# Optimization experiments

Hardware: AMD Instinct MI355X
Metric: run time of the kernel (lower is better)

Reference implementation:

```python
import jax, jax.numpy as jnp
from jax import lax
import numpy as np

N, C, H, W = 8, 128, 96, 96
G, K = 8, 3                      # groups, kernel_size
GC = C // G                      # group channels = 16
STRIDE, PAD, DIL = 1, 1, 1
OFFSET_SCALE = 1.0
OM_DIM = int(np.ceil(G * K * K * 3 / 8) * 8)   # 216 (== G*K*K*3, no padding)
GN_EPS = 1e-5


def setup_inputs() -> dict:
    key = jax.random.key(0)
    ks = jax.random.split(key, 7)
    inp = {
        "input": jax.random.normal(ks[0], (N, C, H, W), dtype=jnp.float32),
        # depthwise conv (Conv2d groups=C): OIHW with I=1
        "dw_w": jax.random.normal(ks[1], (C, 1, K, K), dtype=jnp.float32) * 0.1,
        "dw_b": jax.random.normal(ks[2], (C,), dtype=jnp.float32) * 0.05,
        # GroupNorm(num_groups=1) affine params
        "gn_w": jnp.ones((C,), dtype=jnp.float32),
        "gn_b": jnp.zeros((C,), dtype=jnp.float32),
        # offset_mask Linear (module zero-inits; use small random for a meaningful test)
        "om_w": jax.random.normal(ks[3], (OM_DIM, C), dtype=jnp.float32) * 0.02,
        "om_b": jax.random.normal(ks[4], (OM_DIM,), dtype=jnp.float32) * 0.02,
    }
    return inp


def _dcnv4_forward(x, dw_w, dw_b, gn_w, gn_b, om_w, om_b):
    # x: (N, C, H, W)
    # ---- offset/mask branch: depthwise conv -> GroupNorm(1) -> GELU -> Linear
    x1 = lax.conv_general_dilated(
        x, dw_w, window_strides=(1, 1), padding=[(1, 1), (1, 1)],
        feature_group_count=C, dimension_numbers=("NCHW", "OIHW", "NCHW"))
    x1 = x1 + dw_b[None, :, None, None]
    mu = jnp.mean(x1, axis=(1, 2, 3), keepdims=True)
    var = jnp.var(x1, axis=(1, 2, 3), keepdims=True)
    x1 = (x1 - mu) * lax.rsqrt(var + GN_EPS)
    x1 = x1 * gn_w[None, :, None, None] + gn_b[None, :, None, None]
    x1 = jax.nn.gelu(x1, approximate=False)
    x1 = jnp.transpose(x1, (0, 2, 3, 1))                     # (N,H,W,C)
    om = jnp.einsum("nhwc,oc->nhwo", x1, om_w) + om_b        # (N,H,W,216)

    K2 = K * K
    om = om[..., : G * K2 * 3].reshape(N, H, W, G, K2 * 3)
    offs = om[..., : 2 * K2].reshape(N, H, W, G, K2, 2)      # (dx, dy) per point
    mask = om[..., 2 * K2:]                                  # (N,H,W,G,K2), no softmax in DCNv4

    # ---- sampling locations (pixel coords in the unpadded input, zeros outside)
    ky, kx = jnp.meshgrid(jnp.arange(K), jnp.arange(K), indexing="ij")
    base_y = ((ky - (K - 1) / 2.0) * DIL).reshape(-1).astype(jnp.float32)  # (K2,)
    base_x = ((kx - (K - 1) / 2.0) * DIL).reshape(-1).astype(jnp.float32)
    ctr_y = jnp.arange(H, dtype=jnp.float32) * STRIDE - PAD + DIL * (K - 1) / 2.0
    ctr_x = jnp.arange(W, dtype=jnp.float32) * STRIDE - PAD + DIL * (K - 1) / 2.0
    loc_y = ctr_y[None, :, None, None, None] + (base_y + offs[..., 1]) * OFFSET_SCALE
    loc_x = ctr_x[None, None, :, None, None] + (base_x + offs[..., 0]) * OFFSET_SCALE

    # ---- grouped bilinear gather
    xv = jnp.transpose(x, (0, 2, 3, 1)).reshape(N, H, W, G, GC)   # values, channels-last
    y0 = jnp.floor(loc_y)
    x0 = jnp.floor(loc_x)
    ly = loc_y - y0
    lx = loc_x - x0
    y0i = y0.astype(jnp.int32)
    x0i = x0.astype(jnp.int32)
    n_idx = jnp.arange(N)[:, None, None, None, None]
    g_idx = jnp.arange(G)[None, None, None, :, None]

    def gather(yi, xi):
        valid = (yi >= 0) & (yi < H) & (xi >= 0) & (xi < W)
        yc = jnp.clip(yi, 0, H - 1)
        xc = jnp.clip(xi, 0, W - 1)
        v = xv[n_idx, yc, xc, g_idx]                 # (N,H,W,G,K2,GC)
        return v * valid[..., None].astype(xv.dtype)

    samp = (gather(y0i,     x0i)     * ((1 - ly) * (1 - lx))[..., None]
          + gather(y0i,     x0i + 1) * ((1 - ly) * lx)[..., None]
          + gather(y0i + 1, x0i)     * (ly * (1 - lx))[..., None]
          + gather(y0i + 1, x0i + 1) * (ly * lx)[..., None])

    out = jnp.sum(samp * mask[..., None], axis=4)    # (N,H,W,G,GC)
    out = out.reshape(N, H, W, C)
    return jnp.transpose(out, (0, 3, 1, 2))          # (N,C,H,W)


def reference(input, dw_w, dw_b, gn_w, gn_b, om_w, om_b):
    return _dcnv4_forward(input, dw_w, dw_b, gn_w, gn_b, om_w, om_b)
```

## Files before the change

kernel.cpp:

```cpp
#include <hip/hip_runtime.h>

#define N_   8
#define C_   128
#define H_   96
#define W_   96
#define G_   8
#define GC_  16
#define HW_  (H_ * W_)
#define CHW_ (C_ * HW_)
#define OM_  216
#define OMP_ 224
#define OMROWS2_ 112
#define EPS_ 1e-5f
#define BLKS_PER_N_ 1152

typedef short bf16x8 __attribute__((ext_vector_type(8)));
typedef float f32x4 __attribute__((ext_vector_type(4)));

#if __has_builtin(__builtin_amdgcn_fdot2_f32_bf16)
#define HAVE_DOT2_ 1
typedef __bf16 bf16x2 __attribute__((ext_vector_type(2)));
static __device__ __forceinline__ bf16x2 u2bf2(unsigned int u) {
  union { unsigned int i; bf16x2 v; } c;
  c.i = u;
  return c.v;
}
#else
#define HAVE_DOT2_ 0
#endif

static __device__ __forceinline__ unsigned short f2bf(float f) {
  unsigned int u = __float_as_uint(f);
  unsigned int r = (u + 0x7fffu + ((u >> 16) & 1u)) >> 16;
  return (unsigned short)r;
}
static __device__ __forceinline__ float lo_bf(unsigned int u) {
  return __uint_as_float(u << 16);
}
static __device__ __forceinline__ float hi_bf(unsigned int u) {
  return __uint_as_float(u & 0xffff0000u);
}

static __device__ __forceinline__ float fast_gelu(float z) {
  float s = z * 0.70710678118654752f;
  float as = fabsf(s);
  float t = __builtin_amdgcn_rcpf(fmaf(0.3275911f, as, 1.0f));
  float e = __expf(-as * as);
  float inner = fmaf(fmaf(fmaf(fmaf(1.061405429f, t, -1.453152027f), t,
                               1.421413741f), t, -0.284496736f), t, 0.254829592f);
  float y = fmaf(-inner * t, e, 1.0f);
  float erf_s = copysignf(y, s);
  float hz = 0.5f * z;
  return fmaf(hz, erf_s, hz);
}

__global__ __launch_bounds__(256) void k_front(const float* __restrict__ x,
                                               const float* __restrict__ dw_w,
                                               const float* __restrict__ dw_b,
                                               unsigned short* __restrict__ xgb,
                                               unsigned short* __restrict__ x1b,
                                               float2* __restrict__ partials) {
  __shared__ float tile_c[32][33];
  __shared__ float tile_a[32][33];
  __shared__ float ls[4], lq[4];
  int tx = threadIdx.x;
  int ty = threadIdx.y;
  int p0 = blockIdx.x * 32;
  int c0 = blockIdx.y * 32;
  int n = blockIdx.z;
  int p = p0 + tx;
  int h = p / W_;
  int w = p - h * W_;

  float s = 0.0f, q = 0.0f;
#pragma unroll
  for (int i = 0; i < 4; ++i) {
    int c = c0 + ty + i * 8;
    const float* wp = dw_w + c * 9;
    const float* xp = x + (n * C_ + c) * HW_;
    float acc = dw_b[c];
    float center = 0.0f;
#pragma unroll
    for (int dy = 0; dy < 3; ++dy) {
#pragma unroll
      for (int dx = 0; dx < 3; ++dx) {
        int yy = h + dy - 1;
        int xx = w + dx - 1;
        bool v = (yy >= 0) & (yy < H_) & (xx >= 0) & (xx < W_);
        float xin = v ? xp[yy * W_ + xx] : 0.0f;
        if (dy == 1 && dx == 1) center = xin;
        acc = fmaf(xin, wp[dy * 3 + dx], acc);
      }
    }
    tile_c[ty + i * 8][tx] = center;
    tile_a[ty + i * 8][tx] = acc;
    s += acc;
    q += acc * acc;
  }

  int tid = ty * 32 + tx;
#pragma unroll
  for (int o = 32; o > 0; o >>= 1) {
    s += __shfl_down(s, o);
    q += __shfl_down(q, o);
  }
  int lane = tid & 63;
  int wv = tid >> 6;
  if (lane == 0) { ls[wv] = s; lq[wv] = q; }
  __syncthreads();
  if (tid == 0) {
    int bid = blockIdx.x + 288 * blockIdx.y + BLKS_PER_N_ * n;
    partials[bid] = make_float2(ls[0] + ls[1] + ls[2] + ls[3],
                                lq[0] + lq[1] + lq[2] + lq[3]);
  }

  int c = c0 + tx;
  int g = c >> 4;
  int cc = c & 15;
#pragma unroll
  for (int i = 0; i < 4; ++i) {
    int pp = p0 + ty + i * 8;
    xgb[(((size_t)(n * G_ + g) * HW_) + pp) * GC_ + cc] = f2bf(tile_c[tx][ty + i * 8]);
    x1b[((size_t)(n * HW_) + pp) * C_ + c] = f2bf(tile_a[tx][ty + i * 8]);
  }
}

__global__ __launch_bounds__(256) void k_stats(const float2* __restrict__ partials,
                                               float* __restrict__ stats) {
  int n = blockIdx.x;
  int tid = threadIdx.x;
  const float2* p = partials + n * BLKS_PER_N_;
  float s = 0.0f, q = 0.0f;
  for (int i = tid; i < BLKS_PER_N_; i += 256) {
    float2 v = p[i];
    s += v.x;
    q += v.y;
  }
#pragma unroll
  for (int o = 32; o > 0; o >>= 1) {
    s += __shfl_down(s, o);
    q += __shfl_down(q, o);
  }
  __shared__ float ls[4], lq[4];
  int lane = tid & 63;
  int wv = tid >> 6;
  if (lane == 0) { ls[wv] = s; lq[wv] = q; }
  __syncthreads();
  if (tid == 0) {
    stats[n * 2 + 0] = ls[0] + ls[1] + ls[2] + ls[3];
    stats[n * 2 + 1] = lq[0] + lq[1] + lq[2] + lq[3];
  }
}

__global__ __launch_bounds__(256) void k_prep(const float* __restrict__ om_w,
                                              const float* __restrict__ om_b,
                                              unsigned short* __restrict__ A,
                                              float* __restrict__ biasp) {
  int idx = blockIdx.x * 256 + threadIdx.x;
  int o = idx >> 7;
  int cix = idx & 127;
  int g = o / 28;
  int k = o - g * 28;
  float v = (k < 27) ? om_w[(g * 27 + k) * C_ + cix] : 0.0f;
  A[idx] = f2bf(v);
  if (cix == 0) biasp[o] = (k < 27) ? om_b[g * 27 + k] : 0.0f;
}

__global__ __launch_bounds__(256) void k_gemm_mfma(const unsigned short* __restrict__ Bt,
                                                   const unsigned short* __restrict__ A,
                                                   const float* __restrict__ biasp,
                                                   const float* __restrict__ stats,
                                                   const float* __restrict__ gn_w,
                                                   const float* __restrict__ gn_b,
                                                   unsigned int* __restrict__ om2) {
  __shared__ unsigned short Bl[32 * 136];
  __shared__ alignas(16) float s_bias[OMP_];
  int tid = threadIdx.x;
  int pb = blockIdx.x;
  int n = blockIdx.y;
  int p0 = pb * 32;

  if (tid < OMP_ / 4) {
    ((float4*)s_bias)[tid] = ((const float4*)biasp)[tid];
  }

  float sum = stats[n * 2 + 0];
  float ssq = stats[n * 2 + 1];
  const float inv = 1.0f / (float)CHW_;
  float mean = sum * inv;
  float var = ssq * inv - mean * mean;
  float rstd = rsqrtf(var + EPS_);
  int cbase = (tid & 15) * 8;
  float a8[8], b8[8];
#pragma unroll
  for (int j = 0; j < 8; ++j) {
    float gw = gn_w[cbase + j];
    float gb = gn_b[cbase + j];
    a8[j] = rstd * gw;
    b8[j] = gb - mean * rstd * gw;
  }

  const unsigned short* src = Bt + ((size_t)n * HW_ + p0) * C_;
#pragma unroll
  for (int i = 0; i < 2; ++i) {
    int idx = i * 256 + tid;
    int row = idx >> 4;
    int col = idx & 15;
    uint4 raw = *(const uint4*)(src + row * C_ + col * 8);
    unsigned int d[4] = {raw.x, raw.y, raw.z, raw.w};
    unsigned int od[4];
#pragma unroll
    for (int t = 0; t < 4; ++t) {
      float v0 = lo_bf(d[t]);
      float v1 = hi_bf(d[t]);
      float z0 = fmaf(v0, a8[2 * t], b8[2 * t]);
      float z1 = fmaf(v1, a8[2 * t + 1], b8[2 * t + 1]);
      float g0 = fast_gelu(z0);
      float g1 = fast_gelu(z1);
      od[t] = (unsigned int)f2bf(g0) | ((unsigned int)f2bf(g1) << 16);
    }
    uint4 packed = {od[0], od[1], od[2], od[3]};
    *(uint4*)(&Bl[row * 136 + col * 8]) = packed;
  }
  __syncthreads();

  int wave = tid >> 6;
  int lane = tid & 63;
  int quad = lane >> 4;
  int l16 = lane & 15;
  int pixhalf = wave & 1;
  int othalf = wave >> 1;
  int prow = pixhalf * 16 + l16;

  bf16x8 bfrag[4];
#pragma unroll
  for (int kk = 0; kk < 4; ++kk)
    bfrag[kk] = *(const bf16x8*)(&Bl[prow * 136 + kk * 32 + quad * 8]);

  int p = p0 + prow;
  for (int oi = 0; oi < 7; ++oi) {
    int ot = othalf * 7 + oi;
    const unsigned short* Ap = A + (ot * 16 + l16) * C_ + quad * 8;
    bf16x8 afrag[4];
#pragma unroll
    for (int kk = 0; kk < 4; ++kk)
      afrag[kk] = *(const bf16x8*)(Ap + kk * 32);

    f32x4 acc = {0.f, 0.f, 0.f, 0.f};
#pragma unroll
    for (int kk = 0; kk < 4; ++kk)
      acc = __builtin_amdgcn_mfma_f32_16x16x32_bf16(afrag[kk], bfrag[kk], acc, 0, 0, 0);

    int o0 = ot * 16 + quad * 4;
    float4 bv = *(const float4*)(&s_bias[o0]);
    unsigned int pk0 = (unsigned int)f2bf(acc[0] + bv.x) |
                       ((unsigned int)f2bf(acc[1] + bv.y) << 16);
    unsigned int pk1 = (unsigned int)f2bf(acc[2] + bv.z) |
                       ((unsigned int)f2bf(acc[3] + bv.w) << 16);
    unsigned int* Cp = om2 + ((size_t)n * OMROWS2_ + (o0 >> 1)) * HW_ + p;
    Cp[0] = pk0;
    Cp[HW_] = pk1;
  }
}

__global__ __launch_bounds__(256) void k_sample(const unsigned short* __restrict__ xgb,
                                                const unsigned int* __restrict__ om2,
                                                float* __restrict__ out) {
  __shared__ int4 s_wa[9 * 64];

  int tid = threadIdx.x;
  int ord = blockIdx.x;
  int n = ord & 7;
  int t2 = ord >> 3;
  int g = t2 & 7;
  int pb = t2 >> 3;
  int p0 = pb * 64;

  const unsigned int* omb = om2 + ((size_t)n * OMROWS2_ + g * 14) * HW_ + p0;
  for (int j = tid; j < 576; j += 256) {
    int pt = j >> 6;
    int px = j & 63;
    int p = p0 + px;
    int h = p / W_;
    int w = p - h * W_;
    unsigned int od = omb[pt * HW_ + px];
    float offx = lo_bf(od);
    float offy = hi_bf(od);
    unsigned int md = omb[(9 + (pt >> 1)) * HW_ + px];
    float m = (pt & 1) ? hi_bf(md) : lo_bf(md);
    float locy = (float)(h + pt / 3 - 1) + offy;
    float locx = (float)(w + pt % 3 - 1) + offx;
    float y0f = floorf(locy);
    float x0f = floorf(locx);
    float ly = locy - y0f;
    float lx = locx - x0f;
    int y0 = (int)y0f;
    int x0 = (int)x0f;
    int y1 = y0 + 1;
    int x1 = x0 + 1;
    bool vy0 = (y0 >= 0) & (y0 < H_);
    bool vy1 = (y1 >= 0) & (y1 < H_);
    bool vx0 = (x0 >= 0) & (x0 < W_);
    bool vx1 = (x1 >= 0) & (x1 < W_);
    float t0 = (1.0f - ly) * m;
    float t1 = ly * m;
    float u0 = 1.0f - lx;
    float w00 = (vy0 & vx0) ? t0 * u0 : 0.0f;
    float w01 = (vy0 & vx1) ? t0 * lx : 0.0f;
    float w10 = (vy1 & vx0) ? t1 * u0 : 0.0f;
    float w11 = (vy1 & vx1) ? t1 * lx : 0.0f;
    int yc0 = min(max(y0, 0), H_ - 1);
    int yc1 = min(max(y1, 0), H_ - 1);
    int xs  = min(max(x0, 0), W_ - 2);
    int idx0 = min(max(x0, 0), W_ - 1) - xs;
    int idx1 = min(max(x1, 0), W_ - 1) - xs;
    float wr0y0 = (idx0 == 0 ? w00 : 0.0f) + (idx1 == 0 ? w01 : 0.0f);
    float wr1y0 = (idx0 == 1 ? w00 : 0.0f) + (idx1 == 1 ? w01 : 0.0f);
    float wr0y1 = (idx0 == 0 ? w10 : 0.0f) + (idx1 == 0 ? w11 : 0.0f);
    float wr1y1 = (idx0 == 1 ? w10 : 0.0f) + (idx1 == 1 ? w11 : 0.0f);
    int4 wa;
    wa.x = (int)((unsigned int)f2bf(wr0y0) | ((unsigned int)f2bf(wr0y1) << 16));
    wa.y = (int)((unsigned int)f2bf(wr1y0) | ((unsigned int)f2bf(wr1y1) << 16));
    wa.z = (yc0 * W_ + xs) * GC_;
    wa.w = (yc1 * W_ + xs) * GC_;
    s_wa[j] = wa;
  }
  __syncthreads();

  int px_l = tid >> 2;
  int sub = tid & 3;
  int rowhalf = sub >> 1;
  int chunk = sub & 1;
  int p = p0 + px_l;
  const unsigned short* xbb = xgb + ((size_t)(n * G_ + g) * HW_) * GC_;

  float acc[8] = {0, 0, 0, 0, 0, 0, 0, 0};
#pragma unroll
  for (int pt = 0; pt < 9; ++pt) {
    int4 wa = s_wa[pt * 64 + px_l];
    unsigned int aw = (unsigned int)(rowhalf ? wa.y : wa.x);
    uint4 r0 = *(const uint4*)(xbb + wa.z + sub * 8);
    uint4 r1 = *(const uint4*)(xbb + wa.w + sub * 8);
    unsigned int d0[4] = {r0.x, r0.y, r0.z, r0.w};
    unsigned int d1[4] = {r1.x, r1.y, r1.z, r1.w};
#if HAVE_DOT2_
    bf16x2 a2 = u2bf2(aw);
#pragma unroll
    for (int t = 0; t < 4; ++t) {
      unsigned int blo = __builtin_amdgcn_perm(d1[t], d0[t], 0x05040100u);
      unsigned int bhi = __builtin_amdgcn_perm(d1[t], d0[t], 0x07060302u);
      acc[2 * t]     = __builtin_amdgcn_fdot2_f32_bf16(a2, u2bf2(blo), acc[2 * t], false);
      acc[2 * t + 1] = __builtin_amdgcn_fdot2_f32_bf16(a2, u2bf2(bhi), acc[2 * t + 1], false);
    }
#else
    float w0 = lo_bf(aw);
    float w1 = hi_bf(aw);
#pragma unroll
    for (int t = 0; t < 4; ++t) {
      acc[2 * t]     = fmaf(w0, lo_bf(d0[t]), acc[2 * t]);
      acc[2 * t + 1] = fmaf(w0, hi_bf(d0[t]), acc[2 * t + 1]);
      acc[2 * t]     = fmaf(w1, lo_bf(d1[t]), acc[2 * t]);
      acc[2 * t + 1] = fmaf(w1, hi_bf(d1[t]), acc[2 * t + 1]);
    }
#endif
  }

#pragma unroll
  for (int i = 0; i < 8; ++i) acc[i] += __shfl_xor(acc[i], 2);

  int ch = chunk * 8 + rowhalf * 4;
  float* op = out + ((size_t)(n * C_ + g * GC_ + ch)) * HW_ + p;
#pragma unroll
  for (int r = 0; r < 4; ++r) op[r * HW_] = acc[rowhalf * 4 + r];
}

extern "C" void kernel_launch(void* const* d_in, const int* in_sizes, int n_in,
                              void* d_out, int out_size, void* d_ws, size_t ws_size,
                              hipStream_t stream) {
  const float* x    = (const float*)d_in[0];
  const float* dw_w = (const float*)d_in[1];
  const float* dw_b = (const float*)d_in[2];
  const float* gn_w = (const float*)d_in[3];
  const float* gn_b = (const float*)d_in[4];
  const float* om_w = (const float*)d_in[5];
  const float* om_b = (const float*)d_in[6];
  float* out = (float*)d_out;

  unsigned short* xgb = (unsigned short*)d_ws;
  unsigned short* x1b = xgb + (size_t)N_ * CHW_;
  unsigned int* om2 = (unsigned int*)(x1b + (size_t)N_ * CHW_);
  float* stats = (float*)(om2 + (size_t)N_ * OMROWS2_ * HW_);
  float2* partials = (float2*)(stats + 16);
  unsigned short* Abf = (unsigned short*)(partials + N_ * BLKS_PER_N_);
  float* biasp = (float*)(Abf + OMP_ * C_);

  k_front<<<dim3(HW_ / 32, C_ / 32, N_), dim3(32, 8), 0, stream>>>(
      x, dw_w, dw_b, xgb, x1b, partials);
  k_stats<<<N_, 256, 0, stream>>>(partials, stats);
  k_prep<<<(OMP_ * C_) / 256, 256, 0, stream>>>(om_w, om_b, Abf, biasp);
  k_gemm_mfma<<<dim3(HW_ / 32, N_), 256, 0, stream>>>(
      x1b, Abf, biasp, stats, gn_w, gn_b, om2);
  k_sample<<<9216, 256, 0, stream>>>(xgb, om2, out);
}
```

Before: 197.7 us.

## Retile depthwise conv front kernel with row register reuse and merge stats/prep kernels

The front kernel is restructured so each block handles an 8-row strip for one channel group. Each thread computes 3 pixels of 2 channels using a rolling 3-row register window, so each input element is loaded about once instead of 9 times. Results are packed as bf16 pairs in LDS and written as 16-byte vector stores for both the channel-last value buffer and the GEMM input. The stats and weight-prep kernels are merged into one launch to save a launch. The cost is far fewer blocks (768 instead of 9216), more registers per thread, and a larger LDS footprint, which may hurt occupancy.

New measurement: 189.7 us. 1.04x faster.

```diff
diff --git a/kernel.cpp b/kernel.cpp
--- a/kernel.cpp
+++ b/kernel.cpp
@@ -12,7 +12,7 @@
 #define OMP_ 224
 #define OMROWS2_ 112
 #define EPS_ 1e-5f
-#define BLKS_PER_N_ 1152
+#define BLKS_PER_N_ 96
 
 typedef short bf16x8 __attribute__((ext_vector_type(8)));
 typedef float f32x4 __attribute__((ext_vector_type(4)));
@@ -54,51 +54,117 @@
   return fmaf(hz, erf_s, hz);
 }
 
+static __device__ __forceinline__ void loadrow5(float dst[2][5],
+                                                const float* __restrict__ xp0,
+                                                const float* __restrict__ xp1,
+                                                int hh, int w0) {
+  bool vy = (hh >= 0) & (hh < H_);
+#pragma unroll
+  for (int j = 0; j < 5; ++j) {
+    int ww = w0 - 1 + j;
+    bool v = vy & (ww >= 0) & (ww < W_);
+    dst[0][j] = v ? xp0[hh * W_ + ww] : 0.0f;
+    dst[1][j] = v ? xp1[hh * W_ + ww] : 0.0f;
+  }
+}
+
 __global__ __launch_bounds__(256) void k_front(const float* __restrict__ x,
                                                const float* __restrict__ dw_w,
                                                const float* __restrict__ dw_b,
                                                unsigned short* __restrict__ xgb,
                                                unsigned short* __restrict__ x1b,
                                                float2* __restrict__ partials) {
-  __shared__ float tile_c[32][33];
-  __shared__ float tile_a[32][33];
+  __shared__ unsigned int lds_c[384 * 9];
+  __shared__ unsigned int lds_a[384 * 9];
   __shared__ float ls[4], lq[4];
+
   int tx = threadIdx.x;
   int ty = threadIdx.y;
-  int p0 = blockIdx.x * 32;
-  int c0 = blockIdx.y * 32;
-  int n = blockIdx.z;
-  int p = p0 + tx;
-  int h = p / W_;
-  int w = p - h * W_;
+  int tid = ty * 32 + tx;
+  int hb = blockIdx.x;
+  int g  = blockIdx.y;
+  int n  = blockIdx.z;
+  int h0 = hb * 8;
+  int w0 = tx * 3;
+
+  const int c0 = g * 16 + 2 * ty;
+  float wk[2][9];
+  const float* wp = dw_w + c0 * 9;
+#pragma unroll
+  for (int j = 0; j < 9; ++j) {
+    wk[0][j] = wp[j];
+    wk[1][j] = wp[9 + j];
+  }
+  float bias[2] = {dw_b[c0], dw_b[c0 + 1]};
+
+  const float* xp0 = x + ((size_t)(n * C_ + c0)) * HW_;
+  const float* xp1 = xp0 + HW_;
 
   float s = 0.0f, q = 0.0f;
-#pragma unroll
-  for (int i = 0; i < 4; ++i) {
-    int c = c0 + ty + i * 8;
-    const float* wp = dw_w + c * 9;
-    const float* xp = x + (n * C_ + c) * HW_;
-    float acc = dw_b[c];
-    float center = 0.0f;
-#pragma unroll
-    for (int dy = 0; dy < 3; ++dy) {
-#pragma unroll
-      for (int dx = 0; dx < 3; ++dx) {
-        int yy = h + dy - 1;
-        int xx = w + dx - 1;
-        bool v = (yy >= 0) & (yy < H_) & (xx >= 0) & (xx < W_);
-        float xin = v ? xp[yy * W_ + xx] : 0.0f;
-        if (dy == 1 && dx == 1) center = xin;
-        acc = fmaf(xin, wp[dy * 3 + dx], acc);
+
+#pragma unroll
+  for (int half = 0; half < 2; ++half) {
+    if (half) __syncthreads();
+    int hh0 = h0 + half * 4;
+
+    float rr[3][2][5];
+    loadrow5(rr[0], xp0, xp1, hh0 - 1, w0);
+    loadrow5(rr[1], xp0, xp1, hh0,     w0);
+
+#pragma unroll
+    for (int r = 0; r < 4; ++r) {
+      const int sA = r % 3;
+      const int sB = (r + 1) % 3;
+      const int sC = (r + 2) % 3;
+      loadrow5(rr[sC], xp0, xp1, hh0 + r + 1, w0);
+
+#pragma unroll
+      for (int j = 0; j < 3; ++j) {
+        float acc0 = bias[0], acc1 = bias[1];
+#pragma unroll
+        for (int dx = 0; dx < 3; ++dx) {
+          acc0 = fmaf(rr[sA][0][j + dx], wk[0][0 + dx], acc0);
+          acc1 = fmaf(rr[sA][1][j + dx], wk[1][0 + dx], acc1);
+          acc0 = fmaf(rr[sB][0][j + dx], wk[0][3 + dx], acc0);
+          acc1 = fmaf(rr[sB][1][j + dx], wk[1][3 + dx], acc1);
+          acc0 = fmaf(rr[sC][0][j + dx], wk[0][6 + dx], acc0);
+          acc1 = fmaf(rr[sC][1][j + dx], wk[1][6 + dx], acc1);
+        }
+        float cen0 = rr[sB][0][j + 1];
+        float cen1 = rr[sB][1][j + 1];
+        s += acc0 + acc1;
+        q = fmaf(acc0, acc0, q);
+        q = fmaf(acc1, acc1, q);
+        int pxl = r * 96 + w0 + j;
+        lds_a[pxl * 9 + ty] = (unsigned int)f2bf(acc0) |
+                              ((unsigned int)f2bf(acc1) << 16);
+        lds_c[pxl * 9 + ty] = (unsigned int)f2bf(cen0) |
+                              ((unsigned int)f2bf(cen1) << 16);
       }
     }
-    tile_c[ty + i * 8][tx] = center;
-    tile_a[ty + i * 8][tx] = acc;
-    s += acc;
-    q += acc * acc;
-  }
-
-  int tid = ty * 32 + tx;
+    __syncthreads();
+
+    for (int i = tid; i < 384; i += 256) {
+      int p = h0 * W_ + half * 384 + i;
+      unsigned int wc[8], wa[8];
+#pragma unroll
+      for (int k = 0; k < 8; ++k) {
+        wc[k] = lds_c[i * 9 + k];
+        wa[k] = lds_a[i * 9 + k];
+      }
+      unsigned int* xg = (unsigned int*)xgb + ((size_t)(n * G_ + g) * HW_ + p) * 8;
+      uint4 c01 = {wc[0], wc[1], wc[2], wc[3]};
+      uint4 c23 = {wc[4], wc[5], wc[6], wc[7]};
+      *(uint4*)xg = c01;
+      *(uint4*)(xg + 4) = c23;
+      unsigned int* xb = (unsigned int*)x1b + ((size_t)n * HW_ + p) * 64 + g * 8;
+      uint4 a01 = {wa[0], wa[1], wa[2], wa[3]};
+      uint4 a23 = {wa[4], wa[5], wa[6], wa[7]};
+      *(uint4*)xb = a01;
+      *(uint4*)(xb + 4) = a23;
+    }
+  }
+
 #pragma unroll
   for (int o = 32; o > 0; o >>= 1) {
     s += __shfl_down(s, o);
@@ -109,61 +175,53 @@
   if (lane == 0) { ls[wv] = s; lq[wv] = q; }
   __syncthreads();
   if (tid == 0) {
-    int bid = blockIdx.x + 288 * blockIdx.y + BLKS_PER_N_ * n;
+    int bid = hb + 12 * g + BLKS_PER_N_ * n;
     partials[bid] = make_float2(ls[0] + ls[1] + ls[2] + ls[3],
                                 lq[0] + lq[1] + lq[2] + lq[3]);
   }
-
-  int c = c0 + tx;
-  int g = c >> 4;
-  int cc = c & 15;
-#pragma unroll
-  for (int i = 0; i < 4; ++i) {
-    int pp = p0 + ty + i * 8;
-    xgb[(((size_t)(n * G_ + g) * HW_) + pp) * GC_ + cc] = f2bf(tile_c[tx][ty + i * 8]);
-    x1b[((size_t)(n * HW_) + pp) * C_ + c] = f2bf(tile_a[tx][ty + i * 8]);
-  }
-}
-
-__global__ __launch_bounds__(256) void k_stats(const float2* __restrict__ partials,
-                                               float* __restrict__ stats) {
-  int n = blockIdx.x;
+}
+
+__global__ __launch_bounds__(256) void k_stats_prep(const float2* __restrict__ partials,
+                                                    float* __restrict__ stats,
+                                                    const float* __restrict__ om_w,
+                                                    const float* __restrict__ om_b,
+                                                    unsigned short* __restrict__ A,
+                                                    float* __restrict__ biasp) {
+  __shared__ float ls[4], lq[4];
+  int b = blockIdx.x;
   int tid = threadIdx.x;
-  const float2* p = partials + n * BLKS_PER_N_;
-  float s = 0.0f, q = 0.0f;
-  for (int i = tid; i < BLKS_PER_N_; i += 256) {
-    float2 v = p[i];
-    s += v.x;
-    q += v.y;
-  }
-#pragma unroll
-  for (int o = 32; o > 0; o >>= 1) {
-    s += __shfl_down(s, o);
-    q += __shfl_down(q, o);
-  }
-  __shared__ float ls[4], lq[4];
-  int lane = tid & 63;
-  int wv = tid >> 6;
-  if (lane == 0) { ls[wv] = s; lq[wv] = q; }
-  __syncthreads();
-  if (tid == 0) {
-    stats[n * 2 + 0] = ls[0] + ls[1] + ls[2] + ls[3];
-    stats[n * 2 + 1] = lq[0] + lq[1] + lq[2] + lq[3];
-  }
-}
-
-__global__ __launch_bounds__(256) void k_prep(const float* __restrict__ om_w,
-                                              const float* __restrict__ om_b,
-                                              unsigned short* __restrict__ A,
-                                              float* __restrict__ biasp) {
-  int idx = blockIdx.x * 256 + threadIdx.x;
-  int o = idx >> 7;
-  int cix = idx & 127;
-  int g = o / 28;
-  int k = o - g * 28;
-  float v = (k < 27) ? om_w[(g * 27 + k) * C_ + cix] : 0.0f;
-  A[idx] = f2bf(v);
-  if (cix == 0) biasp[o] = (k < 27) ? om_b[g * 27 + k] : 0.0f;
+  if (b < N_) {
+    int n = b;
+    const float2* p = partials + n * BLKS_PER_N_;
+    float s = 0.0f, q = 0.0f;
+    if (tid < BLKS_PER_N_) {
+      float2 v = p[tid];
+      s = v.x;
+      q = v.y;
+    }
+#pragma unroll
+    for (int o = 32; o > 0; o >>= 1) {
+      s += __shfl_down(s, o);
+      q += __shfl_down(q, o);
+    }
+    int lane = tid & 63;
+    int wv = tid >> 6;
+    if (lane == 0) { ls[wv] = s; lq[wv] = q; }
+    __syncthreads();
+    if (tid == 0) {
+      stats[n * 2 + 0] = ls[0] + ls[1] + ls[2] + ls[3];
+      stats[n * 2 + 1] = lq[0] + lq[1] + lq[2] + lq[3];
+    }
+  } else {
+    int idx = (b - N_) * 256 + tid;
+    int o = idx >> 7;
+    int cix = idx & 127;
+    int gg = o / 28;
+    int k = o - gg * 28;
+    float v = (k < 27) ? om_w[(gg * 27 + k) * C_ + cix] : 0.0f;
+    A[idx] = f2bf(v);
+    if (cix == 0) biasp[o] = (k < 27) ? om_b[gg * 27 + k] : 0.0f;
+  }
 }
 
 __global__ __launch_bounds__(256) void k_gemm_mfma(const unsigned short* __restrict__ Bt,
@@ -394,10 +452,9 @@
   unsigned short* Abf = (unsigned short*)(partials + N_ * BLKS_PER_N_);
   float* biasp = (float*)(Abf + OMP_ * C_);
 
-  k_front<<<dim3(HW_ / 32, C_ / 32, N_), dim3(32, 8), 0, stream>>>(
+  k_front<<<dim3(12, G_, N_), dim3(32, 8), 0, stream>>>(
       x, dw_w, dw_b, xgb, x1b, partials);
-  k_stats<<<N_, 256, 0, stream>>>(partials, stats);
-  k_prep<<<(OMP_ * C_) / 256, 256, 0, stream>>>(om_w, om_b, Abf, biasp);
+  k_stats_prep<<<N_ + 112, 256, 0, stream>>>(partials, stats, om_w, om_b, Abf, biasp);
   k_gemm_mfma<<<dim3(HW_ / 32, N_), 256, 0, stream>>>(
       x1b, Abf, biasp, stats, gn_w, gn_b, om2);
   k_sample<<<9216, 256, 0, stream>>>(xgb, om2, out);
```
